# Optimization experiments

Measured on AMD Instinct MI355X. Metric: run time of the kernel, lower is better.

## Reference

```python
import jax, jax.numpy as jnp
import numpy as np

NUM_CLASSES = 21
EPS = 1e-6
MOMENTUM = 0.99
K_WEAK = 16
K_STRONG = 256
PROB_THRESH = 0.95
IGNORE = 255
NEG = -1e30


def _normalize(x, axis=-1):
    # matches F.normalize(p=2) / CosineSimilarity with eps=1e-6
    n = jnp.linalg.norm(x, axis=axis, keepdims=True)
    return x / jnp.maximum(n, EPS)


def setup_inputs() -> dict:
    key = jax.random.key(0)
    k0, k1, k2, k3, k4, k5 = jax.random.split(key, 6)
    B, C, H, W = 8, 256, 128, 128
    feature_weak = jax.random.normal(k0, (B, C, H, W), jnp.float32)
    feature_strong = jax.random.normal(k1, (B, C, H, W), jnp.float32)
    probablity_weak = jax.random.uniform(k2, (B, H, W), jnp.float32)
    memory_bank = jax.random.normal(k3, (NUM_CLASSES, 1, C), jnp.float32)
    pred_weak = jax.random.randint(k4, (B, H, W), 0, NUM_CLASSES)
    ignore_mask = jax.random.randint(k5, (B, H, W), 0, 256)
    return {
        'feature_weak': feature_weak,
        'feature_strong': feature_strong,
        'probablity_weak': probablity_weak,
        'memory_bank': memory_bank,
        'pred_weak': pred_weak,
        'ignore_mask': ignore_mask,
    }


def reference(feature_weak, feature_strong, probablity_weak, memory_bank, pred_weak, ignore_mask):
    B, C, H, W = feature_weak.shape
    N = B * H * W
    fw = feature_weak.transpose(0, 2, 3, 1).reshape(N, C)   # weak pixel feats
    fs = feature_strong.transpose(0, 2, 3, 1).reshape(N, C) # strong pixel feats
    seg = pred_weak.reshape(N)
    ign = ignore_mask.reshape(N)  # same-size bilinear resize (align_corners) is identity
    prob = probablity_weak.reshape(N)

    valid = ign != IGNORE
    conf = valid & (prob > PROB_THRESH)

    cls = jnp.arange(NUM_CLASSES)
    is_cls = seg[None, :] == cls[:, None]        # [K, N]
    m_weak = is_cls & conf[None, :]              # per-class high-confidence mask
    m_strong = is_cls & valid[None, :]
    n_weak = m_weak.sum(axis=1)                  # [K]
    n_strong = m_strong.sum(axis=1)

    protos = memory_bank[:, 0, :]                # [K, C]
    pn = _normalize(protos)
    sim_w = _normalize(fw) @ pn.T                # [N, K] cos(pixel_weak, proto)
    sim_s = _normalize(fs) @ pn.T                # [N, K] cos(pixel_strong, proto)

    sw = jnp.where(m_weak, sim_w.T, NEG)         # [K, N]
    ss = jnp.where(m_strong, -sim_s.T, NEG)      # negate -> bottom-k via top_k
    _, idx_w = jax.lax.top_k(sw, K_WEAK)         # [K, 16] most-similar weak pixels
    _, idx_s = jax.lax.top_k(ss, K_STRONG)       # [K, 256] least-similar strong pixels

    # select_feature duplicates the top element: slots are ranks [0,0,1,...,14]
    ranks = jnp.maximum(jnp.arange(K_WEAK) - 1, 0)
    sel_w = fw[idx_w[:, ranks]]                  # [K, 16, C]
    sel_s = fs[idx_s]                            # [K, 256, C]

    kw = jnp.minimum(K_WEAK, n_weak)
    ks = jnp.minimum(K_STRONG, n_strong)
    valid_w = jnp.arange(K_WEAK)[None, :] < kw[:, None]     # [K, 16]
    valid_s = jnp.arange(K_STRONG)[None, :] < ks[:, None]   # [K, 256]

    # calculate_loss: weak side detached, max over strong dim, sum / strong count
    wn = _normalize(jax.lax.stop_gradient(sel_w))
    sn = _normalize(sel_s)
    cosm = jnp.einsum('kwc,ksc->kws', wn, sn)    # [K, 16, 256]
    cosm = jnp.where(valid_s[:, None, :], cosm, NEG)
    max_sim = jnp.where(valid_w, cosm.max(axis=2), 0.0)     # [K, 16]
    class_ok = (n_weak > 0) & (n_strong > 0)
    sim_sum = jnp.where(class_ok, max_sim.sum(axis=1), 0.0).sum()
    count = jnp.where(class_ok, ks, 0).sum()
    loss = jnp.where(count > 0, 1.0 - sim_sum / count, 0.0)

    # update_memory: per-class mean of high-confidence weak feats, EMA scatter
    fw_ng = jax.lax.stop_gradient(fw)            # .data copy -> no grad
    wsum = m_weak.astype(fw.dtype) @ fw_ng       # [K, C] segmented sum
    mean = wsum / jnp.maximum(n_weak, 1).astype(fw.dtype)[:, None]
    new_protos = jnp.where((n_weak > 0)[:, None],
                           MOMENTUM * protos + (1.0 - MOMENTUM) * mean,
                           protos)
    new_memory_bank = new_protos[:, None, :]     # [K, 1, C]
    return loss, new_memory_bank
```

## Files before the change

kernel.cpp:

```cpp
#include <hip/hip_runtime.h>
#include <stdint.h>

#define NCLS  21
#define CDIM  256
#define HWSZ  16384
#define NPIX  131072
#define EPSV  1e-6f
#define NEGV  -1e30f
#define CAP_W 4096
#define CAP_S 16384
#define KSEL  256
#define NCC   8
#define CCH   (CDIM/NCC)
#define NPART 8
#define NBLK  (NPIX/1024)

__device__ __forceinline__ uint64_t pack_key(float v, unsigned idx) {
  unsigned u = __float_as_uint(v);
  u = (u & 0x80000000u) ? ~u : (u | 0x80000000u);
  return ((uint64_t)(~u) << 32) | (uint64_t)idx;
}

__global__ void k0_init(const float* __restrict__ mb, float* pn, float* wsum) {
  int k = blockIdx.x, t = threadIdx.x;
  float v = mb[k * CDIM + t];
  float s = v * v;
  for (int o = 32; o > 0; o >>= 1) s += __shfl_down(s, o, 64);
  __shared__ float wsh[4];
  int wid = t >> 6, lane = t & 63;
  if (lane == 0) wsh[wid] = s;
  __syncthreads();
  float tot = wsh[0] + wsh[1] + wsh[2] + wsh[3];
  float inv = 1.0f / fmaxf(sqrtf(tot), EPSV);
  pn[k * CDIM + t] = v * inv;
  wsum[k * CDIM + t] = 0.0f;
}

__global__ void k1a_stream(const float* __restrict__ fw, const float* __restrict__ fs,
                           const float* __restrict__ prob, const int* __restrict__ seg,
                           const int* __restrict__ ign, const float* __restrict__ pn,
                           float* part, float* wsum, int* cnts) {
  __shared__ float pnT[CCH * NCLS];
  __shared__ float wloc[NCLS * (CCH + 1)];
  __shared__ int hs[NCLS], hw2[NCLS];
  int t = threadIdx.x;
  int pg = blockIdx.x;
  int cc = blockIdx.y;
  int c0 = cc * CCH;
  for (int i = t; i < CCH * NCLS; i += 256) {
    int c = i / NCLS, k = i % NCLS;
    pnT[i] = pn[k * CDIM + c0 + c];
  }
  for (int i = t; i < NCLS * (CCH + 1); i += 256) wloc[i] = 0.0f;
  if (cc == 0) {
    for (int i = t; i < NCLS; i += 256) { hs[i] = 0; hw2[i] = 0; }
  }
  __syncthreads();

  int n0 = pg * 1024 + t * 4;
  int b = n0 >> 14, hw = n0 & (HWSZ - 1);
  int4   sg = *(const int4*)(seg + n0);
  int4   ig = *(const int4*)(ign + n0);
  float4 pr = *(const float4*)(prob + n0);
  bool v0 = (ig.x != 255), v1 = (ig.y != 255), v2 = (ig.z != 255), v3 = (ig.w != 255);
  bool cf0 = v0 && (pr.x > 0.95f);
  bool cf1 = v1 && (pr.y > 0.95f);
  bool cf2 = v2 && (pr.z > 0.95f);
  bool cf3 = v3 && (pr.w > 0.95f);
  if (cc == 0) {
    if (v0) atomicAdd(&hs[sg.x], 1);
    if (v1) atomicAdd(&hs[sg.y], 1);
    if (v2) atomicAdd(&hs[sg.z], 1);
    if (v3) atomicAdd(&hs[sg.w], 1);
    if (cf0) atomicAdd(&hw2[sg.x], 1);
    if (cf1) atomicAdd(&hw2[sg.y], 1);
    if (cf2) atomicAdd(&hw2[sg.z], 1);
    if (cf3) atomicAdd(&hw2[sg.w], 1);
  }

  const float* fwp = fw + ((size_t)b * CDIM + c0) * HWSZ + hw;
  const float* fsp = fs + ((size_t)b * CDIM + c0) * HWSZ + hw;

  float4 dw = {0,0,0,0}, nw = {0,0,0,0}, dsv = {0,0,0,0}, ns = {0,0,0,0};
#pragma unroll 4
  for (int cl = 0; cl < CCH; ++cl) {
    float4 a = *(const float4*)(fwp + (size_t)cl * HWSZ);
    float4 s = *(const float4*)(fsp + (size_t)cl * HWSZ);
    float p0 = pnT[cl * NCLS + sg.x];
    float p1 = pnT[cl * NCLS + sg.y];
    float p2 = pnT[cl * NCLS + sg.z];
    float p3 = pnT[cl * NCLS + sg.w];
    dw.x = fmaf(a.x, p0, dw.x); nw.x = fmaf(a.x, a.x, nw.x);
    dw.y = fmaf(a.y, p1, dw.y); nw.y = fmaf(a.y, a.y, nw.y);
    dw.z = fmaf(a.z, p2, dw.z); nw.z = fmaf(a.z, a.z, nw.z);
    dw.w = fmaf(a.w, p3, dw.w); nw.w = fmaf(a.w, a.w, nw.w);
    dsv.x = fmaf(s.x, p0, dsv.x); ns.x = fmaf(s.x, s.x, ns.x);
    dsv.y = fmaf(s.y, p1, dsv.y); ns.y = fmaf(s.y, s.y, ns.y);
    dsv.z = fmaf(s.z, p2, dsv.z); ns.z = fmaf(s.z, s.z, ns.z);
    dsv.w = fmaf(s.w, p3, dsv.w); ns.w = fmaf(s.w, s.w, ns.w);
    if (cf0) atomicAdd(&wloc[sg.x * (CCH + 1) + cl], a.x);
    if (cf1) atomicAdd(&wloc[sg.y * (CCH + 1) + cl], a.y);
    if (cf2) atomicAdd(&wloc[sg.z * (CCH + 1) + cl], a.z);
    if (cf3) atomicAdd(&wloc[sg.w * (CCH + 1) + cl], a.w);
  }
  float4* pp = (float4*)part + ((size_t)cc * NPIX + n0);
  pp[0] = make_float4(dw.x, nw.x, dsv.x, ns.x);
  pp[1] = make_float4(dw.y, nw.y, dsv.y, ns.y);
  pp[2] = make_float4(dw.z, nw.z, dsv.z, ns.z);
  pp[3] = make_float4(dw.w, nw.w, dsv.w, ns.w);

  __syncthreads();
  for (int i = t; i < NCLS * CCH; i += 256) {
    int k = i / CCH, cl = i % CCH;
    float v = wloc[k * (CCH + 1) + cl];
    if (v != 0.0f) atomicAdd(&wsum[k * CDIM + c0 + cl], v);
  }
  if (cc == 0) {
    for (int i = t; i < NCLS; i += 256) {
      cnts[pg * NCLS + i] = hs[i];
      cnts[NBLK * NCLS + pg * NCLS + i] = hw2[i];
    }
  }
}

__global__ void ks_scan(const int* __restrict__ cnts, int* offs, int* scnt, int* wcnt) {
  __shared__ int L[2 * NBLK * NCLS];
  int t = threadIdx.x;
  for (int i = t; i < 2 * NBLK * NCLS; i += 256) L[i] = cnts[i];
  __syncthreads();
  if (t < 2 * NCLS) {
    int q = t % NCLS;
    int typ = t / NCLS;
    int base = typ * NBLK * NCLS;
    int run = 0;
    for (int b2 = 0; b2 < NBLK; ++b2) {
      int v = L[base + b2 * NCLS + q];
      L[base + b2 * NCLS + q] = run;
      run += v;
    }
    if (typ == 0) scnt[q] = run; else wcnt[q] = run;
  }
  __syncthreads();
  for (int i = t; i < 2 * NBLK * NCLS; i += 256) offs[i] = L[i];
}

__global__ void k1b_write(const float* __restrict__ part, const float* __restrict__ prob,
                          const int* __restrict__ seg, const int* __restrict__ ign,
                          const int* __restrict__ offs, uint64_t* wkeys, uint64_t* skeys) {
  __shared__ int ls[NCLS], lw[NCLS];
  int t = threadIdx.x, pg = blockIdx.x;
  if (t < NCLS) {
    ls[t] = offs[pg * NCLS + t];
    lw[t] = offs[NBLK * NCLS + pg * NCLS + t];
  }
  __syncthreads();
  int n0 = pg * 1024 + t * 4;
  int4   sg = *(const int4*)(seg + n0);
  int4   ig = *(const int4*)(ign + n0);
  float4 pr = *(const float4*)(prob + n0);
  float dw[4] = {0,0,0,0}, nw[4] = {0,0,0,0}, ds[4] = {0,0,0,0}, ns[4] = {0,0,0,0};
#pragma unroll
  for (int cc = 0; cc < NCC; ++cc) {
    const float4* pp = (const float4*)part + ((size_t)cc * NPIX + n0);
#pragma unroll
    for (int i = 0; i < 4; ++i) {
      float4 v = pp[i];
      dw[i] += v.x; nw[i] += v.y; ds[i] += v.z; ns[i] += v.w;
    }
  }
  int   sga[4] = {sg.x, sg.y, sg.z, sg.w};
  int   iga[4] = {ig.x, ig.y, ig.z, ig.w};
  float pra[4] = {pr.x, pr.y, pr.z, pr.w};
#pragma unroll
  for (int i = 0; i < 4; ++i) {
    if (iga[i] != 255) {
      int q = sga[i];
      float sim_s = ds[i] / fmaxf(sqrtf(ns[i]), EPSV);
      int pos = atomicAdd(&ls[q], 1);
      if (pos < CAP_S) skeys[(size_t)q * CAP_S + pos] = pack_key(-sim_s, (unsigned)(n0 + i));
      if (pra[i] > 0.95f) {
        float sim_w = dw[i] / fmaxf(sqrtf(nw[i]), EPSV);
        int pw = atomicAdd(&lw[q], 1);
        if (pw < CAP_W) wkeys[(size_t)q * CAP_W + pw] = pack_key(sim_w, (unsigned)(n0 + i));
      }
    }
  }
}

__device__ void select_topk(const uint64_t* __restrict__ list, int cnt,
                            uint64_t* T, uint64_t* P, int* pcnt, int* woff) {
  int t = threadIdx.x;
  T[t] = ~0ull;
  if (t == 0) *pcnt = 0;
  __syncthreads();
  for (int base = 0; base < cnt; base += 256) {
    uint64_t key = (base + t < cnt) ? list[base + t] : ~0ull;
    uint64_t cutoff = T[KSEL - 1];
    bool pred = key < cutoff;
    unsigned long long mask = __ballot(pred);
    int wid = t >> 6, lane = t & 63;
    if (lane == 0) woff[wid] = __popcll(mask);
    int prefix = __popcll(mask & ((1ull << lane) - 1ull));
    __syncthreads();
    int off = 0;
    for (int w2 = 0; w2 < wid; ++w2) off += woff[w2];
    int total = woff[0] + woff[1] + woff[2] + woff[3];
    int old = *pcnt;
    if (pred) P[old + off + prefix] = key;
    int newc = old + total;
    __syncthreads();
    if (t == 0) *pcnt = newc;
    bool last = (base + 256 >= cnt);
    if (newc >= KSEL || (last && newc > 0)) {
      for (int i2 = t; i2 < 2 * KSEL; i2 += 256)
        if (i2 >= newc) P[i2] = ~0ull;
      for (unsigned size = 2; size <= 2 * KSEL; size <<= 1) {
        for (unsigned stride = size >> 1; stride > 0; stride >>= 1) {
          __syncthreads();
          unsigned lo = stride - 1;
          unsigned i = (((unsigned)t & ~lo) << 1) | ((unsigned)t & lo);
          unsigned j = i | stride;
          uint64_t a = P[i], b = P[j];
          bool up = ((i & size) == 0);
          if ((a > b) == up) { P[i] = b; P[j] = a; }
        }
      }
      __syncthreads();
      uint64_t a = T[t], b = P[KSEL - 1 - t];
      T[t] = a < b ? a : b;
      for (unsigned stride = KSEL / 2; stride > 0; stride >>= 1) {
        __syncthreads();
        if (((unsigned)t & stride) == 0) {
          uint64_t x = T[t], y = T[t + stride];
          if (x > y) { T[t] = y; T[t + stride] = x; }
        }
      }
      __syncthreads();
      if (t == 0) *pcnt = 0;
      __syncthreads();
    } else {
      __syncthreads();
    }
  }
}

__global__ void k2_topk(const uint64_t* __restrict__ wkeys, const uint64_t* __restrict__ skeys,
                        const int* wcnt, const int* scnt,
                        uint64_t* psel, int* idxw, int* kwv, int* nwv) {
  __shared__ uint64_t T[KSEL];
  __shared__ uint64_t P[2 * KSEL];
  __shared__ int pcnt;
  __shared__ int woff[4];
  int bid = blockIdx.x, t = threadIdx.x;
  if (bid < NCLS * NPART) {
    int k = bid / NPART, p = bid % NPART;
    int cnt = min(scnt[k], CAP_S);
    int chunk = (cnt + NPART - 1) / NPART;
    int lo = p * chunk;
    int hi = min(lo + chunk, cnt);
    int c = hi > lo ? hi - lo : 0;
    select_topk(skeys + (size_t)k * CAP_S + lo, c, T, P, &pcnt, woff);
    psel[((size_t)k * NPART + p) * KSEL + t] = T[t];
  } else {
    int k = bid - NCLS * NPART;
    int cnt_total = wcnt[k];
    int cnt = min(cnt_total, CAP_W);
    select_topk(wkeys + (size_t)k * CAP_W, cnt, T, P, &pcnt, woff);
    if (t < 16) idxw[k * 16 + t] = (int)(unsigned)(T[t] & 0xFFFFFFFFull);
    if (t == 0) { nwv[k] = cnt_total; kwv[k] = min(cnt_total, 16); }
  }
}

__global__ void k2m_merge(const uint64_t* __restrict__ psel, const int* scnt,
                          int* idxs, int* ksv, int* nsv) {
  int k = blockIdx.x, t = threadIdx.x;
  __shared__ uint64_t M[NPART * KSEL];
  for (int i = t; i < NPART * KSEL; i += 256) M[i] = psel[(size_t)k * NPART * KSEL + i];
  for (unsigned size = 2; size <= NPART * KSEL; size <<= 1) {
    for (unsigned stride = size >> 1; stride > 0; stride >>= 1) {
      __syncthreads();
      for (unsigned q = t; q < NPART * KSEL / 2; q += 256) {
        unsigned lo = stride - 1;
        unsigned i = ((q & ~lo) << 1) | (q & lo);
        unsigned j = i | stride;
        uint64_t a = M[i], b = M[j];
        bool up = ((i & size) == 0);
        if ((a > b) == up) { M[i] = b; M[j] = a; }
      }
    }
  }
  __syncthreads();
  idxs[k * KSEL + t] = (int)(unsigned)(M[t] & 0xFFFFFFFFull);
  if (t == 0) { int c = scnt[k]; nsv[k] = c; ksv[k] = c < KSEL ? c : KSEL; }
}

__global__ void k3a_gather(const float* __restrict__ fw, const float* __restrict__ fs,
                           const int* __restrict__ idxw, const int* __restrict__ idxs,
                           const int* __restrict__ kwv, const int* __restrict__ ksv,
                           float* dw_dense, float* ds_dense) {
  int k = blockIdx.y;
  int slot = blockIdx.x;
  int t = threadIdx.x;
  bool strong = slot < KSEL;
  float v = 0.0f;
  int n = 0;
  bool ok;
  if (strong) {
    ok = slot < ksv[k];
    if (ok) n = idxs[k * KSEL + slot];
  } else {
    int i = slot - KSEL;
    ok = i < kwv[k];
    int rank = i > 0 ? i - 1 : 0;
    if (ok) n = idxw[k * 16 + rank];
  }
  if (ok) {
    int b = n >> 14, hw = n & (HWSZ - 1);
    const float* f = strong ? fs : fw;
    v = f[(size_t)(b * CDIM + t) * HWSZ + hw];
  }
  float s = v * v;
  for (int o = 32; o > 0; o >>= 1) s += __shfl_down(s, o, 64);
  __shared__ float wsh[4];
  int wid = t >> 6, lane = t & 63;
  if (lane == 0) wsh[wid] = s;
  __syncthreads();
  float tot = wsh[0] + wsh[1] + wsh[2] + wsh[3];
  float inv = 1.0f / fmaxf(sqrtf(tot), EPSV);
  float out = v * inv;
  if (strong) ds_dense[((size_t)k * KSEL + slot) * CDIM + t] = out;
  else        dw_dense[((size_t)k * 16 + (slot - KSEL)) * CDIM + t] = out;
}

__global__ void k3b_loss(const float* __restrict__ dw_dense, const float* __restrict__ ds_dense,
                         const int* kwv, const int* ksv, const int* nwv, const int* nsv,
                         float* simsum, int* countk) {
  int k = blockIdx.x, t = threadIdx.x;
  int wid = t >> 6, lane = t & 63;
  __shared__ float wn[16 * CDIM];
  __shared__ float wred[4][16];
  for (int i = t; i < 16 * CDIM; i += 256) wn[i] = dw_dense[(size_t)k * 16 * CDIM + i];
  __syncthreads();
  int ks_ = ksv[k], kw_ = kwv[k];
  bool ok = (nwv[k] > 0) && (nsv[k] > 0);
  float dots[16];
#pragma unroll
  for (int i = 0; i < 16; ++i) dots[i] = 0.0f;
  bool jv = ok && (t < ks_);
  if (jv) {
    const float4* sp = (const float4*)(ds_dense + ((size_t)k * KSEL + t) * CDIM);
    for (int c4 = 0; c4 < CDIM / 4; ++c4) {
      float4 v = sp[c4];
#pragma unroll
      for (int i = 0; i < 16; ++i) {
        float4 w = ((const float4*)(wn + i * CDIM))[c4];
        dots[i] = fmaf(v.x, w.x, dots[i]);
        dots[i] = fmaf(v.y, w.y, dots[i]);
        dots[i] = fmaf(v.z, w.z, dots[i]);
        dots[i] = fmaf(v.w, w.w, dots[i]);
      }
    }
  }
#pragma unroll
  for (int i = 0; i < 16; ++i) {
    float v = jv ? dots[i] : NEGV;
    for (int o = 32; o > 0; o >>= 1) v = fmaxf(v, __shfl_down(v, o, 64));
    if (lane == 0) wred[wid][i] = v;
  }
  __syncthreads();
  if (t == 0) {
    float csum = 0.0f;
    for (int i = 0; i < kw_; ++i) {
      float m = fmaxf(fmaxf(wred[0][i], wred[1][i]), fmaxf(wred[2][i], wred[3][i]));
      csum += m;
    }
    simsum[k] = ok ? csum : 0.0f;
    countk[k] = ok ? ks_ : 0;
  }
}

__global__ void k4_final(const float* __restrict__ mb, const float* __restrict__ wsum,
                         const int* __restrict__ nwv, const float* __restrict__ simsum,
                         const int* __restrict__ countk, float* out) {
  int k = blockIdx.x, t = threadIdx.x;
  float p = mb[k * CDIM + t];
  float o = p;
  int nw = nwv[k];
  if (nw > 0) {
    float mean = wsum[k * CDIM + t] / (float)nw;
    o = 0.99f * p + 0.01f * mean;
  }
  out[1 + k * CDIM + t] = o;
  if (k == 0 && t == 0) {
    float ss = 0.0f;
    int cc = 0;
    for (int q = 0; q < NCLS; ++q) { ss += simsum[q]; cc += countk[q]; }
    out[0] = (cc > 0) ? (1.0f - ss / (float)cc) : 0.0f;
  }
}

extern "C" void kernel_launch(void* const* d_in, const int* in_sizes, int n_in,
                              void* d_out, int out_size, void* d_ws, size_t ws_size,
                              hipStream_t stream) {
  const float* fw   = (const float*)d_in[0];
  const float* fs   = (const float*)d_in[1];
  const float* prob = (const float*)d_in[2];
  const float* mb   = (const float*)d_in[3];
  const int*   seg  = (const int*)d_in[4];
  const int*   ign  = (const int*)d_in[5];
  float* out = (float*)d_out;

  char* ws = (char*)d_ws;
  size_t off = 0;
  auto alloc = [&](size_t bytes) -> char* {
    char* p = ws + off;
    off = (off + bytes + 255) & ~(size_t)255;
    return p;
  };
  float*    pn       = (float*)alloc(NCLS * CDIM * 4);
  float*    wsum     = (float*)alloc(NCLS * CDIM * 4);
  int*      wcnt     = (int*)alloc(NCLS * 4);
  int*      scnt     = (int*)alloc(NCLS * 4);
  int*      idxw     = (int*)alloc(NCLS * 16 * 4);
  int*      idxs     = (int*)alloc(NCLS * KSEL * 4);
  int*      kwv      = (int*)alloc(NCLS * 4);
  int*      ksv      = (int*)alloc(NCLS * 4);
  int*      nwv      = (int*)alloc(NCLS * 4);
  int*      nsv      = (int*)alloc(NCLS * 4);
  float*    simsum   = (float*)alloc(NCLS * 4);
  int*      countk   = (int*)alloc(NCLS * 4);
  int*      cnts     = (int*)alloc(2 * NBLK * NCLS * 4);
  int*      offs     = (int*)alloc(2 * NBLK * NCLS * 4);
  uint64_t* wkeys    = (uint64_t*)alloc((size_t)NCLS * CAP_W * 8);
  uint64_t* skeys    = (uint64_t*)alloc((size_t)NCLS * CAP_S * 8);
  uint64_t* psel     = (uint64_t*)alloc((size_t)NCLS * NPART * KSEL * 8);
  float*    dw_dense = (float*)alloc((size_t)NCLS * 16 * CDIM * 4);
  float*    ds_dense = (float*)alloc((size_t)NCLS * KSEL * CDIM * 4);
  float*    part     = (float*)alloc((size_t)NCC * NPIX * 4 * 4);
  (void)in_sizes; (void)n_in; (void)out_size; (void)ws_size;

  k0_init<<<NCLS, 256, 0, stream>>>(mb, pn, wsum);
  k1a_stream<<<dim3(NBLK, NCC), 256, 0, stream>>>(fw, fs, prob, seg, ign, pn,
                                                  part, wsum, cnts);
  ks_scan<<<1, 256, 0, stream>>>(cnts, offs, scnt, wcnt);
  k1b_write<<<NBLK, 256, 0, stream>>>(part, prob, seg, ign, offs, wkeys, skeys);
  k2_topk<<<NCLS * NPART + NCLS, 256, 0, stream>>>(wkeys, skeys, wcnt, scnt,
                                                   psel, idxw, kwv, nwv);
  k2m_merge<<<NCLS, 256, 0, stream>>>(psel, scnt, idxs, ksv, nsv);
  k3a_gather<<<dim3(KSEL + 16, NCLS), 256, 0, stream>>>(fw, fs, idxw, idxs, kwv, ksv,
                                                        dw_dense, ds_dense);
  k3b_loss<<<NCLS, 256, 0, stream>>>(dw_dense, ds_dense, kwv, ksv, nwv, nsv,
                                     simsum, countk);
  k4_final<<<NCLS, 256, 0, stream>>>(mb, wsum, nwv, simsum, countk, out);
}
```

Measured before the change: 433.6 us.

## Move weak segmented sum to sparse gather kernel and split class counting out

The per-class weak feature sum no longer runs in the main streaming kernel through shared-memory atomics. A separate kernel now sums only the high-confidence pixels listed in the weak key lists, gathering their feature columns. Class histogram counting moves into its own small kernel. The channel split doubles to 16 with a fully unrolled inner loop, and the dense gather buffers reuse the partial buffer to save memory. The streaming kernel becomes lighter, at the cost of two extra launches, strided gathers in the new sum kernel, and a partial buffer that is now twice as large.

```diff
diff --git a/kernel.cpp b/kernel.cpp
--- a/kernel.cpp
+++ b/kernel.cpp
@@ -10,9 +10,10 @@
 #define CAP_W 4096
 #define CAP_S 16384
 #define KSEL  256
-#define NCC   8
+#define NCC   16
 #define CCH   (CDIM/NCC)
 #define NPART 8
+#define NWP   8
 #define NBLK  (NPIX/1024)
 
 __device__ __forceinline__ uint64_t pack_key(float v, unsigned idx) {
@@ -36,13 +37,31 @@
   wsum[k * CDIM + t] = 0.0f;
 }
 
+__global__ void kcount(const int* __restrict__ seg, const int* __restrict__ ign,
+                       const float* __restrict__ prob, int* cnts) {
+  __shared__ int hs[NCLS], hw2[NCLS];
+  int t = threadIdx.x, pg = blockIdx.x;
+  if (t < NCLS) { hs[t] = 0; hw2[t] = 0; }
+  __syncthreads();
+  int n0 = pg * 1024 + t * 4;
+  int4   sg = *(const int4*)(seg + n0);
+  int4   ig = *(const int4*)(ign + n0);
+  float4 pr = *(const float4*)(prob + n0);
+  if (ig.x != 255) { atomicAdd(&hs[sg.x], 1); if (pr.x > 0.95f) atomicAdd(&hw2[sg.x], 1); }
+  if (ig.y != 255) { atomicAdd(&hs[sg.y], 1); if (pr.y > 0.95f) atomicAdd(&hw2[sg.y], 1); }
+  if (ig.z != 255) { atomicAdd(&hs[sg.z], 1); if (pr.z > 0.95f) atomicAdd(&hw2[sg.z], 1); }
+  if (ig.w != 255) { atomicAdd(&hs[sg.w], 1); if (pr.w > 0.95f) atomicAdd(&hw2[sg.w], 1); }
+  __syncthreads();
+  if (t < NCLS) {
+    cnts[pg * NCLS + t] = hs[t];
+    cnts[NBLK * NCLS + pg * NCLS + t] = hw2[t];
+  }
+}
+
 __global__ void k1a_stream(const float* __restrict__ fw, const float* __restrict__ fs,
-                           const float* __restrict__ prob, const int* __restrict__ seg,
-                           const int* __restrict__ ign, const float* __restrict__ pn,
-                           float* part, float* wsum, int* cnts) {
+                           const int* __restrict__ seg, const float* __restrict__ pn,
+                           float* part) {
   __shared__ float pnT[CCH * NCLS];
-  __shared__ float wloc[NCLS * (CCH + 1)];
-  __shared__ int hs[NCLS], hw2[NCLS];
   int t = threadIdx.x;
   int pg = blockIdx.x;
   int cc = blockIdx.y;
@@ -51,38 +70,17 @@
     int c = i / NCLS, k = i % NCLS;
     pnT[i] = pn[k * CDIM + c0 + c];
   }
-  for (int i = t; i < NCLS * (CCH + 1); i += 256) wloc[i] = 0.0f;
-  if (cc == 0) {
-    for (int i = t; i < NCLS; i += 256) { hs[i] = 0; hw2[i] = 0; }
-  }
   __syncthreads();
 
   int n0 = pg * 1024 + t * 4;
   int b = n0 >> 14, hw = n0 & (HWSZ - 1);
-  int4   sg = *(const int4*)(seg + n0);
-  int4   ig = *(const int4*)(ign + n0);
-  float4 pr = *(const float4*)(prob + n0);
-  bool v0 = (ig.x != 255), v1 = (ig.y != 255), v2 = (ig.z != 255), v3 = (ig.w != 255);
-  bool cf0 = v0 && (pr.x > 0.95f);
-  bool cf1 = v1 && (pr.y > 0.95f);
-  bool cf2 = v2 && (pr.z > 0.95f);
-  bool cf3 = v3 && (pr.w > 0.95f);
-  if (cc == 0) {
-    if (v0) atomicAdd(&hs[sg.x], 1);
-    if (v1) atomicAdd(&hs[sg.y], 1);
-    if (v2) atomicAdd(&hs[sg.z], 1);
-    if (v3) atomicAdd(&hs[sg.w], 1);
-    if (cf0) atomicAdd(&hw2[sg.x], 1);
-    if (cf1) atomicAdd(&hw2[sg.y], 1);
-    if (cf2) atomicAdd(&hw2[sg.z], 1);
-    if (cf3) atomicAdd(&hw2[sg.w], 1);
-  }
+  int4 sg = *(const int4*)(seg + n0);
 
   const float* fwp = fw + ((size_t)b * CDIM + c0) * HWSZ + hw;
   const float* fsp = fs + ((size_t)b * CDIM + c0) * HWSZ + hw;
 
   float4 dw = {0,0,0,0}, nw = {0,0,0,0}, dsv = {0,0,0,0}, ns = {0,0,0,0};
-#pragma unroll 4
+#pragma unroll
   for (int cl = 0; cl < CCH; ++cl) {
     float4 a = *(const float4*)(fwp + (size_t)cl * HWSZ);
     float4 s = *(const float4*)(fsp + (size_t)cl * HWSZ);
@@ -98,29 +96,12 @@
     dsv.y = fmaf(s.y, p1, dsv.y); ns.y = fmaf(s.y, s.y, ns.y);
     dsv.z = fmaf(s.z, p2, dsv.z); ns.z = fmaf(s.z, s.z, ns.z);
     dsv.w = fmaf(s.w, p3, dsv.w); ns.w = fmaf(s.w, s.w, ns.w);
-    if (cf0) atomicAdd(&wloc[sg.x * (CCH + 1) + cl], a.x);
-    if (cf1) atomicAdd(&wloc[sg.y * (CCH + 1) + cl], a.y);
-    if (cf2) atomicAdd(&wloc[sg.z * (CCH + 1) + cl], a.z);
-    if (cf3) atomicAdd(&wloc[sg.w * (CCH + 1) + cl], a.w);
   }
   float4* pp = (float4*)part + ((size_t)cc * NPIX + n0);
   pp[0] = make_float4(dw.x, nw.x, dsv.x, ns.x);
   pp[1] = make_float4(dw.y, nw.y, dsv.y, ns.y);
   pp[2] = make_float4(dw.z, nw.z, dsv.z, ns.z);
   pp[3] = make_float4(dw.w, nw.w, dsv.w, ns.w);
-
-  __syncthreads();
-  for (int i = t; i < NCLS * CCH; i += 256) {
-    int k = i / CCH, cl = i % CCH;
-    float v = wloc[k * (CCH + 1) + cl];
-    if (v != 0.0f) atomicAdd(&wsum[k * CDIM + c0 + cl], v);
-  }
-  if (cc == 0) {
-    for (int i = t; i < NCLS; i += 256) {
-      cnts[pg * NCLS + i] = hs[i];
-      cnts[NBLK * NCLS + pg * NCLS + i] = hw2[i];
-    }
-  }
 }
 
 __global__ void ks_scan(const int* __restrict__ cnts, int* offs, int* scnt, int* wcnt) {
@@ -185,6 +166,21 @@
       }
     }
   }
+}
+
+__global__ void kwsum(const float* __restrict__ fw, const uint64_t* __restrict__ wkeys,
+                      const int* __restrict__ wcnt, float* wsum) {
+  int q = blockIdx.x, p = blockIdx.y, t = threadIdx.x;
+  int cnt = min(wcnt[q], CAP_W);
+  int chunk = (cnt + NWP - 1) / NWP;
+  int lo = p * chunk, hi = min(lo + chunk, cnt);
+  float acc = 0.0f;
+  for (int i = lo; i < hi; ++i) {
+    unsigned n = (unsigned)(wkeys[(size_t)q * CAP_W + i] & 0xFFFFFFFFull);
+    int b = (int)(n >> 14), hw = (int)(n & (HWSZ - 1));
+    acc += fw[((size_t)b * CDIM + t) * HWSZ + hw];
+  }
+  if (hi > lo) atomicAdd(&wsum[q * CDIM + t], acc);
 }
 
 __device__ void select_topk(const uint64_t* __restrict__ list, int cnt,
@@ -434,16 +430,17 @@
   uint64_t* wkeys    = (uint64_t*)alloc((size_t)NCLS * CAP_W * 8);
   uint64_t* skeys    = (uint64_t*)alloc((size_t)NCLS * CAP_S * 8);
   uint64_t* psel     = (uint64_t*)alloc((size_t)NCLS * NPART * KSEL * 8);
-  float*    dw_dense = (float*)alloc((size_t)NCLS * 16 * CDIM * 4);
-  float*    ds_dense = (float*)alloc((size_t)NCLS * KSEL * CDIM * 4);
   float*    part     = (float*)alloc((size_t)NCC * NPIX * 4 * 4);
+  float*    dw_dense = part;
+  float*    ds_dense = part + (size_t)NCLS * 16 * CDIM;
   (void)in_sizes; (void)n_in; (void)out_size; (void)ws_size;
 
   k0_init<<<NCLS, 256, 0, stream>>>(mb, pn, wsum);
-  k1a_stream<<<dim3(NBLK, NCC), 256, 0, stream>>>(fw, fs, prob, seg, ign, pn,
-                                                  part, wsum, cnts);
+  kcount<<<NBLK, 256, 0, stream>>>(seg, ign, prob, cnts);
   ks_scan<<<1, 256, 0, stream>>>(cnts, offs, scnt, wcnt);
+  k1a_stream<<<dim3(NBLK, NCC), 256, 0, stream>>>(fw, fs, seg, pn, part);
   k1b_write<<<NBLK, 256, 0, stream>>>(part, prob, seg, ign, offs, wkeys, skeys);
+  kwsum<<<dim3(NCLS, NWP), 256, 0, stream>>>(fw, wkeys, wcnt, wsum);
   k2_topk<<<NCLS * NPART + NCLS, 256, 0, stream>>>(wkeys, skeys, wcnt, scnt,
                                                    psel, idxw, kwv, nwv);
   k2m_merge<<<NCLS, 256, 0, stream>>>(psel, scnt, idxs, ksv, nsv);
```

Result: slower. 486.3 us (+12.2%).
